# Optimization experiments

Hardware: AMD Instinct MI355X
Metric: run time of the kernel (lower is better)

## Reference

```python
import jax, jax.numpy as jnp
import numpy as np

B, T, D = 2, 2048, 2048
H, KV = 32, 8
HD = D // H            # 64
N_REP = H // KV        # 4


def setup_inputs() -> dict:
    key = jax.random.key(0)
    ks = jax.random.split(key, 5)
    x = jax.random.normal(ks[0], (B, T, D), dtype=jnp.float32)
    # RoPE frequencies: angle[t, i] = t / 10000^(2i/HD), i in [0, HD/2)
    inv_freq = 1.0 / (10000.0 ** (jnp.arange(0, HD, 2, dtype=jnp.float32) / HD))
    ang = jnp.arange(T, dtype=jnp.float32)[:, None] * inv_freq[None, :]  # [T, HD/2]
    freqs_cos = jnp.cos(ang)
    freqs_sin = jnp.sin(ang)
    # causal additive mask [1,1,T,T]
    r = jnp.arange(T)
    mask = jnp.where(r[None, :] > r[:, None], -1e9, 0.0).astype(jnp.float32)[None, None]
    s = 0.02
    wq = jax.random.normal(ks[1], (D, H * HD), dtype=jnp.float32) * s
    wk = jax.random.normal(ks[2], (D, KV * HD), dtype=jnp.float32) * s
    wv = jax.random.normal(ks[3], (D, KV * HD), dtype=jnp.float32) * s
    wo = jax.random.normal(ks[4], (H * HD, D), dtype=jnp.float32) * s
    return {"x": x, "freqs_cos": freqs_cos, "freqs_sin": freqs_sin, "mask": mask,
            "wq": wq, "wk": wk, "wv": wv, "wo": wo}


def _rope(t, cos, sin):
    # t: [B, T, h, HD]; complex rotation on consecutive (even, odd) pairs
    t2 = t.reshape(*t.shape[:-1], HD // 2, 2)
    c = cos[None, :, None, :]
    s = sin[None, :, None, :]
    o0 = t2[..., 0] * c - t2[..., 1] * s
    o1 = t2[..., 0] * s + t2[..., 1] * c
    return jnp.stack([o0, o1], axis=-1).reshape(t.shape)


def reference(x, freqs_cos, freqs_sin, mask, wq, wk, wv, wo):
    q = (x @ wq).reshape(B, T, H, HD)
    k = (x @ wk).reshape(B, T, KV, HD)
    v = (x @ wv).reshape(B, T, KV, HD)
    q = _rope(q, freqs_cos, freqs_sin)
    k = _rope(k, freqs_cos, freqs_sin)
    # GQA expand: each kv head repeated N_REP times consecutively
    k = jnp.repeat(k, N_REP, axis=2)  # [B, T, H, HD]
    v = jnp.repeat(v, N_REP, axis=2)
    scores = jnp.einsum('bqhd,bkhd->bhqk', q, k) / jnp.sqrt(jnp.float32(HD))
    scores = scores + mask
    attn = jax.nn.softmax(scores, axis=-1)
    out = jnp.einsum('bhqk,bkhd->bqhd', attn, v).reshape(B, T, H * HD)
    return out @ wo
```

## Files before the change

### kernel.cpp

```cpp
#include <hip/hip_runtime.h>
#include <hip/hip_bf16.h>

#define T_SEQ 2048
#define NROWS 4096
#define QKS   2560

typedef __attribute__((ext_vector_type(8))) short short8;
typedef __attribute__((ext_vector_type(4))) float f32x4;
typedef __attribute__((ext_vector_type(16))) float f32x16;
typedef __attribute__((ext_vector_type(2))) int i32x2;
typedef __attribute__((ext_vector_type(2))) unsigned int u32x2;

#define KC 0.18033688f

__device__ __forceinline__ unsigned short f2bf(float f) {
    unsigned u = __builtin_bit_cast(unsigned, f);
    u += 0x7FFF + ((u >> 16) & 1);
    return (unsigned short)(u >> 16);
}
__device__ __forceinline__ float bf2f(unsigned short s) {
    unsigned u = ((unsigned)s) << 16;
    return __builtin_bit_cast(float, u);
}

__device__ __forceinline__ void gload_lds16(const void* g, void* l) {
    __builtin_amdgcn_global_load_lds(
        (const __attribute__((address_space(1))) unsigned int*)g,
        (__attribute__((address_space(3))) unsigned int*)l,
        16, 0, 0);
}

__device__ __forceinline__ f32x4 mfma16(short8 a, short8 b, f32x4 c) {
    return __builtin_amdgcn_mfma_f32_16x16x32_bf16(a, b, c, 0, 0, 0);
}
__device__ __forceinline__ f32x16 mfma32(short8 a, short8 b, f32x16 c) {
    return __builtin_amdgcn_mfma_f32_32x32x16_bf16(a, b, c, 0, 0, 0);
}

__device__ __forceinline__ unsigned cvtpk_bf16(float lo, float hi) {
    unsigned r;
    asm("v_cvt_pk_bf16_f32 %0, %1, %2" : "=v"(r) : "v"(lo), "v"(hi));
    return r;
}

__device__ __forceinline__ short8 frag_from_u32(unsigned w0, unsigned w1, unsigned w2, unsigned w3) {
    union { unsigned u[4]; short8 s; } t;
    t.u[0] = w0; t.u[1] = w1; t.u[2] = w2; t.u[3] = w3;
    return t.s;
}

__global__ __launch_bounds__(256) void prep(const float* __restrict__ x,
                                            const float* __restrict__ wq,
                                            const float* __restrict__ wk,
                                            const float* __restrict__ wv,
                                            short* __restrict__ xb,
                                            short* __restrict__ wT) {
    __shared__ float tile[32][33];
    const int bid = blockIdx.x, t = threadIdx.x;
    if (bid < 4096) {
        const int i = bid * 256 + t;
        const float4 a = ((const float4*)x)[i * 2];
        const float4 b = ((const float4*)x)[i * 2 + 1];
        ((short8*)xb)[i] = frag_from_u32(cvtpk_bf16(a.x, a.y), cvtpk_bf16(a.z, a.w),
                                         cvtpk_bf16(b.x, b.y), cvtpk_bf16(b.z, b.w));
        return;
    }
    const int r = bid - 4096;
    const int bx = r % 96, by = r / 96;
    const float* S; int srcN, nt, dstRow0;
    if (bx < 64)      { S = wq; srcN = 2048; nt = bx;      dstRow0 = 0;    }
    else if (bx < 80) { S = wk; srcN = 512;  nt = bx - 64; dstRow0 = 2048; }
    else              { S = wv; srcN = 512;  nt = bx - 80; dstRow0 = 2560; }
    const int n0 = nt * 32, k0 = by * 32;
#pragma unroll
    for (int j = 0; j < 4; ++j) {
        int lin = t + 256 * j;
        int kk = lin >> 5, nn = lin & 31;
        tile[kk][nn] = S[(size_t)(k0 + kk) * srcN + n0 + nn];
    }
    __syncthreads();
#pragma unroll
    for (int j = 0; j < 4; ++j) {
        int lin = t + 256 * j;
        int nn = lin >> 5, kk = lin & 31;
        wT[(size_t)(dstRow0 + n0 + nn) * 2048 + k0 + kk] = (short)f2bf(tile[kk][nn]);
    }
}

__global__ __launch_bounds__(256) void transpose_f32_bf16(const float* __restrict__ S,
                                                          short* __restrict__ D,
                                                          int K, int N) {
    __shared__ float tile[32][33];
    const int n0 = blockIdx.x * 32, k0 = blockIdx.y * 32;
    const int t = threadIdx.x;
#pragma unroll
    for (int j = 0; j < 4; ++j) {
        int lin = t + 256 * j;
        int kk = lin >> 5, nn = lin & 31;
        tile[kk][nn] = S[(size_t)(k0 + kk) * N + n0 + nn];
    }
    __syncthreads();
#pragma unroll
    for (int j = 0; j < 4; ++j) {
        int lin = t + 256 * j;
        int nn = lin >> 5, kk = lin & 31;
        D[(size_t)(n0 + nn) * K + k0 + kk] = (short)f2bf(tile[kk][nn]);
    }
}

__global__ __launch_bounds__(256) void rope_vt(unsigned short* __restrict__ qk,
                                               const float* __restrict__ cosp,
                                               const float* __restrict__ sinp,
                                               const short* __restrict__ vbuf,
                                               short* __restrict__ vt) {
    __shared__ short tile[32][33];
    const int bid = blockIdx.x, t = threadIdx.x;
    if (bid < 2048) {
        const int c0 = (bid & 15) * 32, r0 = (bid >> 4) * 32;
#pragma unroll
        for (int j = 0; j < 4; ++j) {
            int lin = t + 256 * j;
            int rr = lin >> 5, cc = lin & 31;
            tile[rr][cc] = vbuf[(size_t)(r0 + rr) * 512 + c0 + cc];
        }
        __syncthreads();
#pragma unroll
        for (int j = 0; j < 4; ++j) {
            int lin = t + 256 * j;
            int cc = lin >> 5, rr = lin & 31;
            vt[(size_t)(c0 + cc) * NROWS + r0 + rr] = tile[rr][cc];
        }
        return;
    }
    int i = (bid - 2048) * 256 + t;
    int Hn = 32, c0 = 0;
    if (i >= 2097152) { i -= 2097152; Hn = 8; c0 = 2048; }
    const int gp = i * 2;
    const int p = gp & 31;
    const int hh = (gp >> 5) % Hn;
    const int row = gp / (32 * Hn);
    const int tpos = row & (T_SEQ - 1);
    const float2 cw = *(const float2*)(cosp + tpos * 32 + p);
    const float2 sw = *(const float2*)(sinp + tpos * 32 + p);
    const size_t base = (size_t)row * QKS + c0 + hh * 64 + 2 * p;
    u32x2 v = *(u32x2*)(qk + base);
    const float e0 = bf2f((unsigned short)(v.x & 0xFFFF)), o0 = bf2f((unsigned short)(v.x >> 16));
    const float e1 = bf2f((unsigned short)(v.y & 0xFFFF)), o1 = bf2f((unsigned short)(v.y >> 16));
    v.x = cvtpk_bf16(e0 * cw.x - o0 * sw.x, e0 * sw.x + o0 * cw.x);
    v.y = cvtpk_bf16(e1 * cw.y - o1 * sw.y, e1 * sw.y + o1 * cw.y);
    *(u32x2*)(qk + base) = v;
}

template <int STORE_F32>
__global__ __launch_bounds__(256) void gemm_mfma(const short* __restrict__ A,
                                                 const short* __restrict__ Bt,
                                                 void* __restrict__ C, int ldc,
                                                 short* __restrict__ Cv, int nsplit,
                                                 int M, int N, int K) {
    __shared__ short As[2][128 * 32];
    __shared__ short Bs[2][128 * 32];
    const int tid = threadIdx.x;
    const int l = tid & 63, w = tid >> 6;
    const int wr = w >> 1, wc = w & 1;
    const int lm = l & 15, lg = l >> 4;

    const int nwg = gridDim.x * gridDim.y;
    int bid = blockIdx.y * gridDim.x + blockIdx.x;
    bid = (bid & 7) * (nwg >> 3) + (bid >> 3);
    const int row0 = (bid / gridDim.x) * 128;
    const int col0 = (bid % gridDim.x) * 128;

    f32x4 acc[4][4];
#pragma unroll
    for (int m = 0; m < 4; ++m)
#pragma unroll
        for (int n = 0; n < 4; ++n) acc[m][n] = (f32x4){0.f, 0.f, 0.f, 0.f};

    auto STAGE = [&](int buf, int kt) {
        const int k0 = kt * 32;
#pragma unroll
        for (int p = 0; p < 2; ++p) {
            const int c = tid + 256 * p;
            const int r = c >> 2, k8 = (c & 3) * 8;
            gload_lds16(A  + (size_t)(row0 + r) * K + k0 + k8, &As[buf][c * 8]);
            gload_lds16(Bt + (size_t)(col0 + r) * K + k0 + k8, &Bs[buf][c * 8]);
        }
    };

    const int nk = K >> 5;
    STAGE(0, 0);
    asm volatile("s_waitcnt vmcnt(0)" ::: "memory");
    __syncthreads();

    for (int kt = 0; kt < nk; ++kt) {
        const int cur = kt & 1;
        if (kt + 1 < nk) STAGE(cur ^ 1, kt + 1);

        short8 af[4], bfr[4];
#pragma unroll
        for (int m = 0; m < 4; ++m)
            af[m] = *(const short8*)(&As[cur][(wr * 64 + m * 16 + lm) * 32 + lg * 8]);
#pragma unroll
        for (int n = 0; n < 4; ++n)
            bfr[n] = *(const short8*)(&Bs[cur][(wc * 64 + n * 16 + lm) * 32 + lg * 8]);
#pragma unroll
        for (int m = 0; m < 4; ++m)
#pragma unroll
            for (int n = 0; n < 4; ++n)
                acc[m][n] = mfma16(af[m], bfr[n], acc[m][n]);

        asm volatile("s_waitcnt vmcnt(0)" ::: "memory");
        __syncthreads();
    }

    const bool vreg = (!STORE_F32) && (col0 >= nsplit);
#pragma unroll
    for (int m = 0; m < 4; ++m)
#pragma unroll
        for (int n = 0; n < 4; ++n) {
            if (vreg) {
#pragma unroll
                for (int r = 0; r < 4; ++r) {
                    const int row = row0 + wr * 64 + m * 16 + lg * 4 + r;
                    const int col = col0 + wc * 64 + n * 16 + lm - nsplit;
                    Cv[(size_t)row * 512 + col] = (short)f2bf(acc[m][n][r]);
                }
            } else {
#pragma unroll
                for (int r = 0; r < 4; ++r) {
                    const int row = row0 + wr * 64 + m * 16 + lg * 4 + r;
                    const int col = col0 + wc * 64 + n * 16 + lm;
                    const float v = acc[m][n][r];
                    if (STORE_F32) ((float*)C)[(size_t)row * ldc + col] = v;
                    else ((unsigned short*)C)[(size_t)row * ldc + col] = f2bf(v);
                }
            }
        }
}

__global__ __launch_bounds__(256, 4) void attn_fwd(const short* __restrict__ qkv,
                                                   const short* __restrict__ vt,
                                                   unsigned short* __restrict__ aout) {
    __shared__ short Ks[2][64 * 64];
    __shared__ short Vs[2][64 * 64];
    const int bid = blockIdx.x;
    const int q2 = (bid & 3) ^ ((bid >> 8) & 3);
    const int t  = (bid >> 2) & 15;
    const int gb = ((bid >> 6) & 3) | (((bid >> 8) & 3) << 2);
    const int qt = (q2 == 0) ? t : (q2 == 1) ? (31 - t) : (q2 == 2) ? (32 + t) : (63 - t);
    const int g = gb & 7, b = gb >> 3;

    const int tid = threadIdx.x, l = tid & 63, w = tid >> 6;
    const int n = l & 31, hi = l >> 5;
    const int h = g * 4 + w;
    const int Q0 = qt * 32;
    const int qg = Q0 + n;

    const size_t krow_base = (size_t)(b * T_SEQ) * QKS + 2048 + g * 64;
    const size_t vrow_base = (size_t)(g * 64) * NROWS + b * T_SEQ;

    short8 qb[4];
    {
        const size_t qbase = (size_t)(b * T_SEQ + qg) * QKS + h * 64 + hi * 8;
        qb[0] = *(const short8*)(qkv + qbase);
        qb[1] = *(const short8*)(qkv + qbase + 16);
        qb[2] = *(const short8*)(qkv + qbase + 32);
        qb[3] = *(const short8*)(qkv + qbase + 48);
    }

    f32x16 acc0 = {}, acc1 = {};
    float m_run = -1e30f, l_run = 0.f;

    const int ntiles = (qt >> 1) + 1;

    auto STAGE = [&](int buf, int kt) {
        const int krow0 = kt * 64;
#pragma unroll
        for (int p = 0; p < 2; ++p) {
            const int c = p * 256 + tid;
            const int r = c >> 3, gk = c & 7;
            const int gs = gk ^ (r & 7);
            gload_lds16(qkv + krow_base + (size_t)(krow0 + r) * QKS + gs * 8,
                        &Ks[buf][c * 8]);
            gload_lds16(vt + vrow_base + (size_t)r * NROWS + krow0 + gs * 8,
                        &Vs[buf][c * 8]);
        }
    };

    STAGE(0, 0);
    asm volatile("s_waitcnt vmcnt(0)" ::: "memory");
    __syncthreads();

    for (int kt = 0; kt < ntiles; ++kt) {
        const int cur = kt & 1;
        if (kt + 1 < ntiles) STAGE(cur ^ 1, kt + 1);

        const int krow0 = kt * 64;
        const short* KsB = &Ks[cur][0];
        const short* VsB = &Vs[cur][0];

        f32x16 s0 = {}, s1 = {};
        __builtin_amdgcn_s_setprio(1);
#pragma unroll
        for (int ks = 0; ks < 4; ++ks) {
            const int perm = ((2 * ks + hi) ^ (n & 7)) * 8;
            const short8 kf0 = *(const short8*)(KsB + n * 64 + perm);
            const short8 kf1 = *(const short8*)(KsB + (32 + n) * 64 + perm);
            s0 = mfma32(kf0, qb[ks], s0);
            s1 = mfma32(kf1, qb[ks], s1);
        }
        __builtin_amdgcn_s_setprio(0);

        if (krow0 + 63 > Q0) {
#pragma unroll
            for (int r = 0; r < 16; ++r) {
                const int jj = krow0 + (r & 3) + 8 * (r >> 2) + 4 * hi;
                if (jj > qg) s0[r] = -1e30f;
                if (jj + 32 > qg) s1[r] = -1e30f;
            }
        }

        float t8[8];
#pragma unroll
        for (int r = 0; r < 8; ++r)
            t8[r] = fmaxf(fmaxf(s0[r], s0[r + 8]), fmaxf(s1[r], s1[r + 8]));
        float mx = fmaxf(fmaxf(fmaxf(t8[0], t8[1]), fmaxf(t8[2], t8[3])),
                         fmaxf(fmaxf(t8[4], t8[5]), fmaxf(t8[6], t8[7])));
        mx = fmaxf(mx, __shfl_xor(mx, 32));
        const float pm = mx * KC;

        if (!__all(pm <= m_run + 8.0f)) {
            const float mn = fmaxf(m_run, pm);
            const float sc = __builtin_amdgcn_exp2f(m_run - mn);
            l_run *= sc;
#pragma unroll
            for (int r = 0; r < 16; ++r) { acc0[r] *= sc; acc1[r] *= sc; }
            m_run = mn;
        }

        float ps[4] = {0.f, 0.f, 0.f, 0.f};
#pragma unroll
        for (int r = 0; r < 16; ++r) {
            const float p = __builtin_amdgcn_exp2f(__builtin_fmaf(s0[r], KC, -m_run));
            s0[r] = p; ps[r & 3] += p;
        }
#pragma unroll
        for (int r = 0; r < 16; ++r) {
            const float p = __builtin_amdgcn_exp2f(__builtin_fmaf(s1[r], KC, -m_run));
            s1[r] = p; ps[r & 3] += p;
        }
        float pst = (ps[0] + ps[1]) + (ps[2] + ps[3]);
        pst += __shfl_xor(pst, 32);
        l_run += pst;

        __builtin_amdgcn_s_setprio(1);
#define PV_STEP(KS, SV)                                                              \
        {                                                                            \
            const unsigned c01 = cvtpk_bf16(SV[((KS)&1)*8+0], SV[((KS)&1)*8+1]);     \
            const unsigned c23 = cvtpk_bf16(SV[((KS)&1)*8+2], SV[((KS)&1)*8+3]);     \
            const unsigned c45 = cvtpk_bf16(SV[((KS)&1)*8+4], SV[((KS)&1)*8+5]);     \
            const unsigned c67 = cvtpk_bf16(SV[((KS)&1)*8+6], SV[((KS)&1)*8+7]);     \
            const i32x2 r02 = __builtin_amdgcn_permlane32_swap((int)c01, (int)c45, false, false); \
            const i32x2 r13 = __builtin_amdgcn_permlane32_swap((int)c23, (int)c67, false, false); \
            const short8 pfrag = frag_from_u32((unsigned)r02.x, (unsigned)r13.x,     \
                                               (unsigned)r02.y, (unsigned)r13.y);    \
            const int permv = ((2 * (KS) + hi) ^ (n & 7)) * 8;                       \
            const short8 vf0 = *(const short8*)(VsB + n * 64 + permv);               \
            const short8 vf1 = *(const short8*)(VsB + (32 + n) * 64 + permv);        \
            acc0 = mfma32(vf0, pfrag, acc0);                                         \
            acc1 = mfma32(vf1, pfrag, acc1);                                         \
        }
        PV_STEP(0, s0)
        PV_STEP(1, s0)
        PV_STEP(2, s1)
        PV_STEP(3, s1)
#undef PV_STEP
        __builtin_amdgcn_s_setprio(0);

        asm volatile("s_waitcnt vmcnt(0)" ::: "memory");
        __syncthreads();
    }

    const float invl = 1.0f / l_run;
    const size_t orow = (size_t)(b * T_SEQ + qg) * 2048 + h * 64;
#pragma unroll
    for (int rg = 0; rg < 4; ++rg) {
        u32x2 pk0, pk1;
        pk0.x = cvtpk_bf16(acc0[rg * 4 + 0] * invl, acc0[rg * 4 + 1] * invl);
        pk0.y = cvtpk_bf16(acc0[rg * 4 + 2] * invl, acc0[rg * 4 + 3] * invl);
        pk1.x = cvtpk_bf16(acc1[rg * 4 + 0] * invl, acc1[rg * 4 + 1] * invl);
        pk1.y = cvtpk_bf16(acc1[rg * 4 + 2] * invl, acc1[rg * 4 + 3] * invl);
        *(u32x2*)(aout + orow + rg * 8 + hi * 4) = pk0;
        *(u32x2*)(aout + orow + 32 + rg * 8 + hi * 4) = pk1;
    }
}

extern "C" void kernel_launch(void* const* d_in, const int* in_sizes, int n_in,
                              void* d_out, int out_size, void* d_ws, size_t ws_size,
                              hipStream_t stream) {
    const float* x    = (const float*)d_in[0];
    const float* fcos = (const float*)d_in[1];
    const float* fsin = (const float*)d_in[2];
    const float* wq   = (const float*)d_in[4];
    const float* wk   = (const float*)d_in[5];
    const float* wv   = (const float*)d_in[6];
    const float* wo   = (const float*)d_in[7];

    short* ws0  = (short*)d_ws;
    short* qkvb = ws0;
    short* vt   = ws0 + 10485760;
    short* wT   = ws0 + 12582912;
    short* vbuf = ws0 + 18874368;
    short* aout = ws0 + 12582912;
    short* woT  = ws0;
    short* xb   = (short*)d_out;

    prep<<<10240, 256, 0, stream>>>(x, wq, wk, wv, xb, wT);
    gemm_mfma<0><<<dim3(24, 32), 256, 0, stream>>>(xb, wT, qkvb, QKS, vbuf, 2560,
                                                   NROWS, 3072, 2048);
    rope_vt<<<12288, 256, 0, stream>>>((unsigned short*)qkvb, fcos, fsin, vbuf, vt);
    attn_fwd<<<1024, 256, 0, stream>>>(qkvb, vt, (unsigned short*)aout);
    transpose_f32_bf16<<<dim3(64, 64), 256, 0, stream>>>(wo, woT, 2048, 2048);
    gemm_mfma<1><<<dim3(16, 32), 256, 0, stream>>>(aout, woT, d_out, 2048, nullptr, 1 << 30,
                                                   NROWS, 2048, 2048);
}
```

Baseline: 209.6 us.

## Use 256x256 8-wave GEMM, fuse Q RoPE into attention, widen attention blocks

Replaces the 128x128 four-wave GEMM with a 256x256 tile, 512-thread kernel using 64-wide K steps, XOR-swizzled LDS and staged half-tile prefetch interleaved with MFMA phases. This raises data reuse per loaded tile and improves overlap. Query RoPE moves into the attention kernel's Q load, so rope_vt only rotates K. Attention now runs 512-thread blocks covering 64 query rows with four K/V LDS slots processed two tiles at a time. The cost is more LDS and registers per block, and fewer blocks for the output GEMM (128 blocks).

```diff
diff --git a/kernel.cpp b/kernel.cpp
--- a/kernel.cpp
+++ b/kernel.cpp
@@ -132,17 +132,15 @@
         }
         return;
     }
-    int i = (bid - 2048) * 256 + t;
-    int Hn = 32, c0 = 0;
-    if (i >= 2097152) { i -= 2097152; Hn = 8; c0 = 2048; }
+    const int i = (bid - 2048) * 256 + t;
     const int gp = i * 2;
     const int p = gp & 31;
-    const int hh = (gp >> 5) % Hn;
-    const int row = gp / (32 * Hn);
+    const int hh = (gp >> 5) & 7;
+    const int row = gp >> 8;
     const int tpos = row & (T_SEQ - 1);
     const float2 cw = *(const float2*)(cosp + tpos * 32 + p);
     const float2 sw = *(const float2*)(sinp + tpos * 32 + p);
-    const size_t base = (size_t)row * QKS + c0 + hh * 64 + 2 * p;
+    const size_t base = (size_t)row * QKS + 2048 + hh * 64 + 2 * p;
     u32x2 v = *(u32x2*)(qk + base);
     const float e0 = bf2f((unsigned short)(v.x & 0xFFFF)), o0 = bf2f((unsigned short)(v.x >> 16));
     const float e1 = bf2f((unsigned short)(v.y & 0xFFFF)), o1 = bf2f((unsigned short)(v.y >> 16));
@@ -152,84 +150,158 @@
 }
 
 template <int STORE_F32>
-__global__ __launch_bounds__(256) void gemm_mfma(const short* __restrict__ A,
-                                                 const short* __restrict__ Bt,
-                                                 void* __restrict__ C, int ldc,
-                                                 short* __restrict__ Cv, int nsplit,
-                                                 int M, int N, int K) {
-    __shared__ short As[2][128 * 32];
-    __shared__ short Bs[2][128 * 32];
+__global__ __launch_bounds__(512, 2) void gemm8(const short* __restrict__ A,
+                                                const short* __restrict__ Bt,
+                                                void* __restrict__ C, int ldc,
+                                                short* __restrict__ Cv, int nsplit,
+                                                int M, int N, int K) {
+    __shared__ short As[2][256 * 64];
+    __shared__ short Bs[2][256 * 64];
     const int tid = threadIdx.x;
     const int l = tid & 63, w = tid >> 6;
-    const int wr = w >> 1, wc = w & 1;
+    const int wm = w >> 2, wn = w & 3;
     const int lm = l & 15, lg = l >> 4;
 
     const int nwg = gridDim.x * gridDim.y;
     int bid = blockIdx.y * gridDim.x + blockIdx.x;
     bid = (bid & 7) * (nwg >> 3) + (bid >> 3);
-    const int row0 = (bid / gridDim.x) * 128;
-    const int col0 = (bid % gridDim.x) * 128;
-
-    f32x4 acc[4][4];
-#pragma unroll
-    for (int m = 0; m < 4; ++m)
+    const int row0 = (bid / gridDim.x) * 256;
+    const int col0 = (bid % gridDim.x) * 256;
+
+    f32x4 acc[8][4];
+#pragma unroll
+    for (int m = 0; m < 8; ++m)
 #pragma unroll
         for (int n = 0; n < 4; ++n) acc[m][n] = (f32x4){0.f, 0.f, 0.f, 0.f};
 
-    auto STAGE = [&](int buf, int kt) {
-        const int k0 = kt * 32;
+    auto STAGE_A = [&](int bb, int h, int kt) {
 #pragma unroll
         for (int p = 0; p < 2; ++p) {
-            const int c = tid + 256 * p;
-            const int r = c >> 2, k8 = (c & 3) * 8;
-            gload_lds16(A  + (size_t)(row0 + r) * K + k0 + k8, &As[buf][c * 8]);
-            gload_lds16(Bt + (size_t)(col0 + r) * K + k0 + k8, &Bs[buf][c * 8]);
+            const int idx = p * 512 + tid;
+            const int band = idx >> 9;
+            const int r = band * 128 + h * 64 + ((idx >> 3) & 63);
+            const int s = idx & 7;
+            const int gsrc = s ^ (r & 7);
+            gload_lds16(A + (size_t)(row0 + r) * K + kt * 64 + gsrc * 8,
+                        &As[bb][band * 8192 + h * 4096 + (idx & 511) * 8]);
         }
     };
-
-    const int nk = K >> 5;
-    STAGE(0, 0);
-    asm volatile("s_waitcnt vmcnt(0)" ::: "memory");
-    __syncthreads();
+    auto STAGE_B = [&](int bb, int h, int kt) {
+#pragma unroll
+        for (int p = 0; p < 2; ++p) {
+            const int idx = p * 512 + tid;
+            const int band = idx >> 8;
+            const int r = band * 64 + h * 32 + ((idx >> 3) & 31);
+            const int s = idx & 7;
+            const int gsrc = s ^ (r & 7);
+            gload_lds16(Bt + (size_t)(col0 + r) * K + kt * 64 + gsrc * 8,
+                        &Bs[bb][band * 4096 + h * 2048 + (idx & 255) * 8]);
+        }
+    };
+
+    short8 a4[4][2], b4[2][2];
+
+#define RD_A(BUF, MH)                                                         \
+    {                                                                         \
+        _Pragma("unroll")                                                     \
+        for (int i = 0; i < 4; ++i)                                           \
+            _Pragma("unroll")                                                 \
+            for (int kh = 0; kh < 2; ++kh) {                                  \
+                const int r = wm * 128 + ((MH) * 4 + i) * 16 + lm;            \
+                const int s = (kh * 4 + lg) ^ (r & 7);                        \
+                a4[i][kh] = *(const short8*)(&As[BUF][r * 64 + s * 8]);       \
+            }                                                                 \
+    }
+#define RD_B(BUF, NH)                                                         \
+    {                                                                         \
+        _Pragma("unroll")                                                     \
+        for (int j = 0; j < 2; ++j)                                           \
+            _Pragma("unroll")                                                 \
+            for (int kh = 0; kh < 2; ++kh) {                                  \
+                const int r = wn * 64 + ((NH) * 2 + j) * 16 + lm;             \
+                const int s = (kh * 4 + lg) ^ (r & 7);                        \
+                b4[j][kh] = *(const short8*)(&Bs[BUF][r * 64 + s * 8]);       \
+            }                                                                 \
+    }
+#define MM(MH, NH)                                                            \
+    {                                                                         \
+        __builtin_amdgcn_s_setprio(1);                                        \
+        _Pragma("unroll")                                                     \
+        for (int i = 0; i < 4; ++i)                                           \
+            _Pragma("unroll")                                                 \
+            for (int j = 0; j < 2; ++j)                                       \
+                _Pragma("unroll")                                             \
+                for (int kh = 0; kh < 2; ++kh)                                \
+                    acc[(MH) * 4 + i][(NH) * 2 + j] =                         \
+                        mfma16(a4[i][kh], b4[j][kh], acc[(MH) * 4 + i][(NH) * 2 + j]); \
+        __builtin_amdgcn_s_setprio(0);                                        \
+    }
+#define VM2  asm volatile("s_waitcnt vmcnt(2)" ::: "memory")
+#define VM0  asm volatile("s_waitcnt vmcnt(0)" ::: "memory")
+#define BAR  __builtin_amdgcn_s_barrier()
+
+    const int nk = K >> 6;
+    STAGE_A(0, 0, 0);
+    STAGE_A(0, 1, 0);
+    STAGE_B(0, 0, 0);
+    STAGE_B(0, 1, 0);
+    VM2;
+    BAR;
 
     for (int kt = 0; kt < nk; ++kt) {
-        const int cur = kt & 1;
-        if (kt + 1 < nk) STAGE(cur ^ 1, kt + 1);
-
-        short8 af[4], bfr[4];
-#pragma unroll
-        for (int m = 0; m < 4; ++m)
-            af[m] = *(const short8*)(&As[cur][(wr * 64 + m * 16 + lm) * 32 + lg * 8]);
-#pragma unroll
-        for (int n = 0; n < 4; ++n)
-            bfr[n] = *(const short8*)(&Bs[cur][(wc * 64 + n * 16 + lm) * 32 + lg * 8]);
-#pragma unroll
-        for (int m = 0; m < 4; ++m)
-#pragma unroll
-            for (int n = 0; n < 4; ++n)
-                acc[m][n] = mfma16(af[m], bfr[n], acc[m][n]);
-
-        asm volatile("s_waitcnt vmcnt(0)" ::: "memory");
-        __syncthreads();
-    }
+        const int buf = kt & 1, nb = buf ^ 1;
+        const bool more = (kt + 1 < nk);
+
+        RD_A(buf, 0); RD_B(buf, 0);
+        if (more) STAGE_A(nb, 0, kt + 1);
+        BAR;
+        MM(0, 0);
+        if (more) VM2; else VM0;
+        BAR;
+
+        RD_B(buf, 1);
+        if (more) STAGE_A(nb, 1, kt + 1);
+        BAR;
+        MM(0, 1);
+        BAR;
+
+        RD_A(buf, 1); RD_B(buf, 0);
+        if (more) STAGE_B(nb, 0, kt + 1);
+        BAR;
+        MM(1, 0);
+        BAR;
+
+        RD_B(buf, 1);
+        if (more) STAGE_B(nb, 1, kt + 1);
+        BAR;
+        MM(1, 1);
+        if (more) VM2; else VM0;
+        BAR;
+    }
+#undef RD_A
+#undef RD_B
+#undef MM
+#undef VM2
+#undef VM0
+#undef BAR
 
     const bool vreg = (!STORE_F32) && (col0 >= nsplit);
 #pragma unroll
-    for (int m = 0; m < 4; ++m)
+    for (int m = 0; m < 8; ++m)
 #pragma unroll
         for (int n = 0; n < 4; ++n) {
             if (vreg) {
 #pragma unroll
                 for (int r = 0; r < 4; ++r) {
-                    const int row = row0 + wr * 64 + m * 16 + lg * 4 + r;
-                    const int col = col0 + wc * 64 + n * 16 + lm - nsplit;
+                    const int row = row0 + wm * 128 + m * 16 + lg * 4 + r;
+                    const int col = col0 + wn * 64 + n * 16 + lm - nsplit;
                     Cv[(size_t)row * 512 + col] = (short)f2bf(acc[m][n][r]);
                 }
             } else {
 #pragma unroll
                 for (int r = 0; r < 4; ++r) {
-                    const int row = row0 + wr * 64 + m * 16 + lg * 4 + r;
-                    const int col = col0 + wc * 64 + n * 16 + lm;
+                    const int row = row0 + wm * 128 + m * 16 + lg * 4 + r;
+                    const int col = col0 + wn * 64 + n * 16 + lm;
                     const float v = acc[m][n][r];
                     if (STORE_F32) ((float*)C)[(size_t)row * ldc + col] = v;
                     else ((unsigned short*)C)[(size_t)row * ldc + col] = f2bf(v);
@@ -238,22 +310,24 @@
         }
 }
 
-__global__ __launch_bounds__(256, 4) void attn_fwd(const short* __restrict__ qkv,
+__global__ __launch_bounds__(512, 4) void attn_fwd(const short* __restrict__ qkv,
                                                    const short* __restrict__ vt,
+                                                   const float* __restrict__ cosp,
+                                                   const float* __restrict__ sinp,
                                                    unsigned short* __restrict__ aout) {
-    __shared__ short Ks[2][64 * 64];
-    __shared__ short Vs[2][64 * 64];
+    __shared__ short Ks[4][64 * 64];
+    __shared__ short Vs[4][64 * 64];
     const int bid = blockIdx.x;
-    const int q2 = (bid & 3) ^ ((bid >> 8) & 3);
-    const int t  = (bid >> 2) & 15;
-    const int gb = ((bid >> 6) & 3) | (((bid >> 8) & 3) << 2);
-    const int qt = (q2 == 0) ? t : (q2 == 1) ? (31 - t) : (q2 == 2) ? (32 + t) : (63 - t);
-    const int g = gb & 7, b = gb >> 3;
+    const int t = (bid >> 1) & 15;
+    const int gbb = (bid >> 5) & 15;
+    const int h1 = (bid & 1) ^ ((bid >> 8) & 1);
+    const int qt = h1 ? (31 - t) : t;
+    const int g = gbb & 7, b = gbb >> 3;
 
     const int tid = threadIdx.x, l = tid & 63, w = tid >> 6;
     const int n = l & 31, hi = l >> 5;
-    const int h = g * 4 + w;
-    const int Q0 = qt * 32;
+    const int h = g * 4 + (w & 3);
+    const int Q0 = qt * 64 + (w >> 2) * 32;
     const int qg = Q0 + n;
 
     const size_t krow_base = (size_t)(b * T_SEQ) * QKS + 2048 + g * 64;
@@ -266,38 +340,42 @@
         qb[1] = *(const short8*)(qkv + qbase + 16);
         qb[2] = *(const short8*)(qkv + qbase + 32);
         qb[3] = *(const short8*)(qkv + qbase + 48);
+#pragma unroll
+        for (int ks = 0; ks < 4; ++ks) {
+            const float4 cw = *(const float4*)(cosp + qg * 32 + ks * 8 + hi * 4);
+            const float4 sw = *(const float4*)(sinp + qg * 32 + ks * 8 + hi * 4);
+            union { short8 s; unsigned u[4]; } f;
+            f.s = qb[ks];
+#pragma unroll
+            for (int j2 = 0; j2 < 4; ++j2) {
+                const float cc = (j2 == 0) ? cw.x : (j2 == 1) ? cw.y : (j2 == 2) ? cw.z : cw.w;
+                const float ss = (j2 == 0) ? sw.x : (j2 == 1) ? sw.y : (j2 == 2) ? sw.z : sw.w;
+                const float e = bf2f((unsigned short)(f.u[j2] & 0xFFFF));
+                const float o = bf2f((unsigned short)(f.u[j2] >> 16));
+                f.u[j2] = cvtpk_bf16(e * cc - o * ss, e * ss + o * cc);
+            }
+            qb[ks] = f.s;
+        }
     }
 
     f32x16 acc0 = {}, acc1 = {};
     float m_run = -1e30f, l_run = 0.f;
 
-    const int ntiles = (qt >> 1) + 1;
-
-    auto STAGE = [&](int buf, int kt) {
+    const int ntiles = qt + 1;
+
+    auto STAGE = [&](int slot, int kt) {
         const int krow0 = kt * 64;
-#pragma unroll
-        for (int p = 0; p < 2; ++p) {
-            const int c = p * 256 + tid;
-            const int r = c >> 3, gk = c & 7;
-            const int gs = gk ^ (r & 7);
-            gload_lds16(qkv + krow_base + (size_t)(krow0 + r) * QKS + gs * 8,
-                        &Ks[buf][c * 8]);
-            gload_lds16(vt + vrow_base + (size_t)r * NROWS + krow0 + gs * 8,
-                        &Vs[buf][c * 8]);
-        }
+        const int c = tid;
+        const int r = c >> 3, gk = c & 7;
+        const int gs = gk ^ (r & 7);
+        gload_lds16(qkv + krow_base + (size_t)(krow0 + r) * QKS + gs * 8,
+                    &Ks[slot][c * 8]);
+        gload_lds16(vt + vrow_base + (size_t)r * NROWS + krow0 + gs * 8,
+                    &Vs[slot][c * 8]);
     };
 
-    STAGE(0, 0);
-    asm volatile("s_waitcnt vmcnt(0)" ::: "memory");
-    __syncthreads();
-
-    for (int kt = 0; kt < ntiles; ++kt) {
-        const int cur = kt & 1;
-        if (kt + 1 < ntiles) STAGE(cur ^ 1, kt + 1);
-
+    auto COMPUTE = [&](int kt, const short* KsB, const short* VsB) {
         const int krow0 = kt * 64;
-        const short* KsB = &Ks[cur][0];
-        const short* VsB = &Vs[cur][0];
 
         f32x16 s0 = {}, s1 = {};
         __builtin_amdgcn_s_setprio(1);
@@ -376,6 +454,21 @@
         PV_STEP(3, s1)
 #undef PV_STEP
         __builtin_amdgcn_s_setprio(0);
+    };
+
+    STAGE(0, 0);
+    if (ntiles > 1) STAGE(1, 1);
+    asm volatile("s_waitcnt vmcnt(0)" ::: "memory");
+    __syncthreads();
+
+    for (int base = 0; base < ntiles; base += 2) {
+        const int pr = (base & 2);
+        const int npr = pr ^ 2;
+        if (base + 2 < ntiles) STAGE(npr, base + 2);
+        if (base + 3 < ntiles) STAGE(npr + 1, base + 3);
+
+        COMPUTE(base, &Ks[pr][0], &Vs[pr][0]);
+        if (base + 1 < ntiles) COMPUTE(base + 1, &Ks[pr + 1][0], &Vs[pr + 1][0]);
 
         asm volatile("s_waitcnt vmcnt(0)" ::: "memory");
         __syncthreads();
@@ -416,11 +509,11 @@
     short* xb   = (short*)d_out;
 
     prep<<<10240, 256, 0, stream>>>(x, wq, wk, wv, xb, wT);
-    gemm_mfma<0><<<dim3(24, 32), 256, 0, stream>>>(xb, wT, qkvb, QKS, vbuf, 2560,
-                                                   NROWS, 3072, 2048);
-    rope_vt<<<12288, 256, 0, stream>>>((unsigned short*)qkvb, fcos, fsin, vbuf, vt);
-    attn_fwd<<<1024, 256, 0, stream>>>(qkvb, vt, (unsigned short*)aout);
+    gemm8<0><<<dim3(12, 16), 512, 0, stream>>>(xb, wT, qkvb, QKS, vbuf, 2560,
+                                               NROWS, 3072, 2048);
+    rope_vt<<<4096, 256, 0, stream>>>((unsigned short*)qkvb, fcos, fsin, vbuf, vt);
+    attn_fwd<<<512, 512, 0, stream>>>(qkvb, vt, fcos, fsin, (unsigned short*)aout);
     transpose_f32_bf16<<<dim3(64, 64), 256, 0, stream>>>(wo, woT, 2048, 2048);
-    gemm_mfma<1><<<dim3(16, 32), 256, 0, stream>>>(aout, woT, d_out, 2048, nullptr, 1 << 30,
-                                                   NROWS, 2048, 2048);
-}
+    gemm8<1><<<dim3(8, 16), 512, 0, stream>>>(aout, woT, d_out, 2048, nullptr, 1 << 30,
+                                              NROWS, 2048, 2048);
+}
```

Measured after the change: 213.7 us. Within noise of the previous version (+1.9%).
